# Kernel optimization log

Hardware: AMD Instinct MI355X
Metric: run time of the kernel (lower is better)

Reference implementation:

```python
import jax, jax.numpy as jnp
import numpy as np

OUT = 8192   # out_features
IN = 8192    # in_features
GS = 64      # HQQ group_size (axis=0 grouping)
NG = OUT * IN // GS   # number of quantization groups = 1048576
B = 64       # tokens in the batch


def setup_inputs() -> dict:
    key = jax.random.key(0)
    k1, k2, k3, k4, k5 = jax.random.split(key, 5)
    x = jax.random.normal(k1, (B, IN), dtype=jnp.float32)
    # packed 4-bit weights: two 4-bit values per byte, packed along axis 0
    # (HQQ pack_4bit_u8: packed = (W[:GS//2] << 4) | W[GS//2:])
    W_q = jax.random.randint(k2, (GS // 2, NG), 0, 256, dtype=jnp.int32)
    scale = jax.random.uniform(k3, (1, NG), dtype=jnp.float32, minval=0.001, maxval=0.02)
    zero = jax.random.uniform(k4, (1, NG), dtype=jnp.float32, minval=0.0, maxval=15.0)
    bias = jax.random.normal(k5, (OUT,), dtype=jnp.float32) * 0.01
    return {"x": x, "W_q": W_q, "scale": scale, "zero": zero, "bias": bias}


def reference(x, W_q, scale, zero, bias):
    # Unpack 4-bit: high nibble holds rows [0, GS//2), low nibble rows [GS//2, GS)
    hi = (W_q >> 4).astype(jnp.float32)          # (GS//2, NG)
    lo = (W_q & 0xF).astype(jnp.float32)         # (GS//2, NG)
    Wu = jnp.concatenate([hi, lo], axis=0)       # (GS, NG)
    # HQQ group-wise dequant: W = (W_q - zero) * scale, then reshape to (out, in)
    W = ((Wu - zero) * scale).reshape(OUT, IN)
    # linear: y = x @ W^T + bias
    return x @ W.T + bias
```

## Files before the change

### kernel.cpp

```cpp
#include <hip/hip_runtime.h>
#include <stdint.h>

#define OUT_F 8192
#define IN_F  8192
#define NGRP  1048576
#define BATCH 64
#define KS    4
#define NSTEP ((IN_F / KS) / 128)

typedef float f32x4  __attribute__((ext_vector_type(4)));
typedef float f32x16 __attribute__((ext_vector_type(16)));
typedef _Float16 half8_t __attribute__((ext_vector_type(8)));

static __device__ __forceinline__ unsigned int pk_fma_f16(unsigned int a, unsigned int b, unsigned int c) {
  unsigned int d;
  asm("v_pk_fma_f16 %0, %1, %2, %3" : "=v"(d) : "v"(a), "v"(b), "v"(c));
  return d;
}
static __device__ __forceinline__ unsigned int pk16(float a, float b) {
  unsigned short ua = __builtin_bit_cast(unsigned short, (_Float16)a);
  unsigned short ub = __builtin_bit_cast(unsigned short, (_Float16)b);
  return (unsigned int)ua | ((unsigned int)ub << 16);
}
static __device__ __forceinline__ unsigned int f2bf_pk(float a, float b) {
  unsigned ua = __builtin_bit_cast(unsigned, a);
  unsigned ub = __builtin_bit_cast(unsigned, b);
  ua = (ua + 0x7fffu + ((ua >> 16) & 1u)) >> 16;
  ub = (ub + 0x7fffu + ((ub >> 16) & 1u)) >> 16;
  return ua | (ub << 16);
}

#define GLL16(g, l)                                                         \
  __builtin_amdgcn_global_load_lds(                                         \
      (const __attribute__((address_space(1))) void*)(g),                   \
      (__attribute__((address_space(3))) void*)(l), 16, 0, 0)

__global__ __launch_bounds__(256) void pre_kernel(const float* __restrict__ x, ushort* __restrict__ xh,
                                                  const float* __restrict__ scale, const float* __restrict__ zero,
                                                  uint32_t* __restrict__ szb) {
  const int b = blockIdx.x;
  if (b < 512) {
    const int i = b * 256 + threadIdx.x;
    float4 v = ((const float4*)x)[i];
    ushort4 o;
    o.x = __builtin_bit_cast(unsigned short, (_Float16)v.x);
    o.y = __builtin_bit_cast(unsigned short, (_Float16)v.y);
    o.z = __builtin_bit_cast(unsigned short, (_Float16)v.z);
    o.w = __builtin_bit_cast(unsigned short, (_Float16)v.w);
    ((ushort4*)xh)[i] = o;
  } else {
    const int i = (b - 512) * 256 + threadIdx.x;
    float4 s = ((const float4*)scale)[i];
    float4 z = ((const float4*)zero)[i];
    uint4 o;
    o.x = pk16(s.x, s.y);
    o.y = pk16(-(64.f + z.x) * s.x, -(64.f + z.y) * s.y);
    o.z = pk16(s.z, s.w);
    o.w = pk16(-(64.f + z.z) * s.z, -(64.f + z.w) * s.w);
    ((uint4*)szb)[i] = o;
  }
}

__global__ __launch_bounds__(512, 4) void hqq_gemm_kernel(
    const int* __restrict__ Wq, const uint32_t* __restrict__ szb,
    const ushort* __restrict__ xh, ushort* __restrict__ partb)
{
  __shared__ ushort xlds[3][64 * 128];
  __shared__ ushort blds[2][64 * 128];

  const int t    = threadIdx.x;
  const int bid  = blockIdx.x;
  const int ks   = bid & 3;
  const int c    = bid >> 2;
  const int lane = t & 63;
  const int wid  = t >> 6;
  const int kbase = ks * (IN_F / KS);

  const int lr = t >> 5;
  const int i0 = (t & 31) * 4;
  const int* __restrict__ wq0 = Wq + (size_t)lr * NGRP + (size_t)c * IN_F + kbase + i0;
  const int* __restrict__ wq1 = wq0 + (size_t)16 * NGRP;
  const uint8_t* __restrict__ szp =
      (const uint8_t*)szb + ((size_t)c * IN_F + kbase + i0) * 4;
  const int wb0 = (i0 * 2) ^ ((lr & 7) << 4);

  const int kh   = wid & 1;
  const int mh   = (wid >> 1) & 1;
  const int nh   = wid >> 2;
  const int ln31 = lane & 31;
  const int koct = lane >> 5;
  const int arow = mh * 32 + ln31;
  const int brow = nh * 32 + ln31;

  f32x16 acc = {0.f, 0.f, 0.f, 0.f, 0.f, 0.f, 0.f, 0.f,
                0.f, 0.f, 0.f, 0.f, 0.f, 0.f, 0.f, 0.f};

  auto stage_x = [&](int bi, int s) {
    #pragma unroll
    for (int j = 0; j < 2; ++j) {
      const int m    = wid * 8 + j * 4 + (lane >> 4);
      const int scol = ((lane & 15) * 16) ^ ((m & 7) << 4);
      const ushort* g = xh + (size_t)m * IN_F + kbase + s * 128 + (scol >> 1);
      GLL16(g, &xlds[bi][(wid * 8 + j * 4) * 128]);
    }
  };

  auto ldregs = [&](int s, int4& w0, int4& w1, uint4& z4) {
    w0 = *(const int4*)(wq0 + (size_t)s * 128);
    w1 = *(const int4*)(wq1 + (size_t)s * 128);
    z4 = *(const uint4*)(szp + (size_t)s * 512);
  };

  auto stage_b = [&](int bi, const int4& w0, const int4& w1, const uint4& z4) {
    uint8_t* bb = (uint8_t*)&blds[bi][0];
    auto dqrow = [&](const int4& wv, int r) {
      unsigned tt0 = ((unsigned)wv.y << 16) | (unsigned)wv.x;
      unsigned tt1 = ((unsigned)wv.w << 16) | (unsigned)wv.z;
      uint2 hh, ll;
      hh.x = pk_fma_f16((tt0 & 0x00F000F0u) | 0x54005400u, z4.x, z4.y);
      hh.y = pk_fma_f16((tt1 & 0x00F000F0u) | 0x54005400u, z4.z, z4.w);
      ll.x = pk_fma_f16(((tt0 << 4) & 0x00F000F0u) | 0x54005400u, z4.x, z4.y);
      ll.y = pk_fma_f16(((tt1 << 4) & 0x00F000F0u) | 0x54005400u, z4.z, z4.w);
      *(uint2*)(bb + r * 256 + wb0)        = hh;
      *(uint2*)(bb + (r + 32) * 256 + wb0) = ll;
    };
    dqrow(w0, lr);
    dqrow(w1, lr + 16);
  };

  {
    int4 a0, a1; uint4 z0;
    ldregs(0, a0, a1, z0);
    stage_b(0, a0, a1, z0);
  }
  stage_x(0, 0);
  stage_x(1, 1);
  int4 w0, w1; uint4 z4;
  ldregs(1, w0, w1, z4);

  int xr0 = 0, xr1 = 1, xr2 = 2;

  #pragma unroll 1
  for (int s = 0; s < NSTEP; ++s) {
    asm volatile("s_waitcnt lgkmcnt(0)" ::: "memory");
    __builtin_amdgcn_s_barrier();

    const bool more2 = (s + 2 < NSTEP);
    int4 n0, n1; uint4 nz;
    if (more2) {
      stage_x(xr2, s + 2);
      ldregs(s + 2, n0, n1, nz);
    }

    if (more2)               asm volatile("s_waitcnt vmcnt(10)" ::: "memory");
    else if (s + 1 < NSTEP)  asm volatile("s_waitcnt vmcnt(5)" ::: "memory");
    else                     asm volatile("s_waitcnt vmcnt(0)" ::: "memory");
    __builtin_amdgcn_sched_barrier(0);

    const uint8_t* xb   = (const uint8_t*)&xlds[xr0][0];
    const uint8_t* bbuf = (const uint8_t*)&blds[s & 1][0];
    #pragma unroll
    for (int j = 0; j < 4; ++j) {
      const int kk   = kh * 4 + j;
      const int colb = (kk * 16 + koct * 8) * 2;
      half8_t a = *(const half8_t*)(xb   + arow * 256 + (colb ^ ((arow & 7) << 4)));
      half8_t b = *(const half8_t*)(bbuf + brow * 256 + (colb ^ ((brow & 7) << 4)));
      acc = __builtin_amdgcn_mfma_f32_32x32x16_f16(a, b, acc, 0, 0, 0);
    }

    if (s + 1 < NSTEP) stage_b((s + 1) & 1, w0, w1, z4);
    if (more2) { w0 = n0; w1 = n1; z4 = nz; }

    const int tmp = xr0; xr0 = xr1; xr1 = xr2; xr2 = tmp;
  }

  __syncthreads();
  float* red = (float*)&blds[0][0];
  {
    float4* dst = (float4*)(red + ((size_t)(wid * 64 + lane)) * 16);
    dst[0] = (float4){acc[0],  acc[1],  acc[2],  acc[3]};
    dst[1] = (float4){acc[4],  acc[5],  acc[6],  acc[7]};
    dst[2] = (float4){acc[8],  acc[9],  acc[10], acc[11]};
    dst[3] = (float4){acc[12], acc[13], acc[14], acc[15]};
  }
  __syncthreads();
  if (kh == 0) {
    const float4* src = (const float4*)(red + ((size_t)((wid ^ 1) * 64 + lane)) * 16);
    float4 p0 = src[0], p1 = src[1], p2 = src[2], p3 = src[3];
    const int o = ln31 * 128 + c + nh * 4096;
    const int mbase = mh * 32 + 4 * koct;
    ushort* bp = partb + ((size_t)ks * OUT_F + o) * BATCH + mbase;
    uint2 q;
    q.x = f2bf_pk(acc[0]  + p0.x, acc[1]  + p0.y);
    q.y = f2bf_pk(acc[2]  + p0.z, acc[3]  + p0.w);
    *(uint2*)(bp + 0) = q;
    q.x = f2bf_pk(acc[4]  + p1.x, acc[5]  + p1.y);
    q.y = f2bf_pk(acc[6]  + p1.z, acc[7]  + p1.w);
    *(uint2*)(bp + 8) = q;
    q.x = f2bf_pk(acc[8]  + p2.x, acc[9]  + p2.y);
    q.y = f2bf_pk(acc[10] + p2.z, acc[11] + p2.w);
    *(uint2*)(bp + 16) = q;
    q.x = f2bf_pk(acc[12] + p3.x, acc[13] + p3.y);
    q.y = f2bf_pk(acc[14] + p3.z, acc[15] + p3.w);
    *(uint2*)(bp + 24) = q;
  }
}

__global__ __launch_bounds__(256) void reduce_kernel(const ushort* __restrict__ partb,
                                                     const float* __restrict__ bias,
                                                     float* __restrict__ out)
{
  __shared__ float tile[32][65];
  const int ob = blockIdx.x;
  const int t  = threadIdx.x;
  {
    const int ol = t >> 3;
    const int mg = t & 7;
    const int o  = ob * 32 + ol;
    const size_t base = (size_t)o * BATCH + mg * 8;
    float s[8] = {0, 0, 0, 0, 0, 0, 0, 0};
    #pragma unroll
    for (int ks = 0; ks < KS; ++ks) {
      const ushort* p = partb + (size_t)ks * OUT_F * BATCH + base;
      uint4 v = *(const uint4*)p;
      s[0] += __uint_as_float(v.x << 16); s[1] += __uint_as_float(v.x & 0xffff0000u);
      s[2] += __uint_as_float(v.y << 16); s[3] += __uint_as_float(v.y & 0xffff0000u);
      s[4] += __uint_as_float(v.z << 16); s[5] += __uint_as_float(v.z & 0xffff0000u);
      s[6] += __uint_as_float(v.w << 16); s[7] += __uint_as_float(v.w & 0xffff0000u);
    }
    const float bv = bias[o];
    #pragma unroll
    for (int j = 0; j < 8; ++j) tile[ol][mg * 8 + j] = s[j] + bv;
  }
  __syncthreads();
  {
    const int m  = t >> 2;
    const int og = (t & 3) * 8;
    float r[8];
    #pragma unroll
    for (int j = 0; j < 8; ++j) r[j] = tile[og + j][m];
    float* op = out + (size_t)m * OUT_F + ob * 32 + og;
    *(float4*)op       = (float4){r[0], r[1], r[2], r[3]};
    *(float4*)(op + 4) = (float4){r[4], r[5], r[6], r[7]};
  }
}

__global__ void hqq_fallback_kernel(const float* __restrict__ x, const int* __restrict__ Wq,
                                    const float* __restrict__ scale, const float* __restrict__ zero,
                                    const float* __restrict__ bias, float* __restrict__ out)
{
  int idx = blockIdx.x * blockDim.x + threadIdx.x;
  int b = idx >> 13;
  int o = idx & 8191;
  int g = o >> 7, cc = o & 127;
  int r = g & 31;
  bool hi = (g < 32);
  const int*   wrow = Wq    + (size_t)r  * NGRP + (size_t)cc * IN_F;
  const float* srow = scale + (size_t)cc * IN_F;
  const float* zrow = zero  + (size_t)cc * IN_F;
  const float* xrow = x     + (size_t)b  * IN_F;
  float acc = 0.f;
  for (int k = 0; k < IN_F; ++k) {
    int v = wrow[k];
    float nib = (float)(hi ? (v >> 4) : (v & 15));
    acc += xrow[k] * ((nib - zrow[k]) * srow[k]);
  }
  out[idx] = acc + bias[o];
}

extern "C" void kernel_launch(void* const* d_in, const int* in_sizes, int n_in,
                              void* d_out, int out_size, void* d_ws, size_t ws_size,
                              hipStream_t stream) {
  const float* x     = (const float*)d_in[0];
  const int*   Wq    = (const int*)d_in[1];
  const float* scale = (const float*)d_in[2];
  const float* zero  = (const float*)d_in[3];
  const float* bias  = (const float*)d_in[4];
  float* out = (float*)d_out;

  const size_t xh_bytes   = (size_t)BATCH * IN_F * sizeof(ushort);
  const size_t sz_bytes   = (size_t)NGRP * 4;
  const size_t part_bytes = (size_t)KS * BATCH * OUT_F * sizeof(ushort);

  if (ws_size >= xh_bytes + sz_bytes + part_bytes) {
    ushort*   xh    = (ushort*)d_ws;
    uint32_t* szb   = (uint32_t*)((char*)d_ws + xh_bytes);
    ushort*   partb = (ushort*)((char*)d_ws + xh_bytes + sz_bytes);
    pre_kernel<<<1536, 256, 0, stream>>>(x, xh, scale, zero, szb);
    hqq_gemm_kernel<<<128 * KS, 512, 0, stream>>>(Wq, szb, xh, partb);
    reduce_kernel<<<OUT_F / 32, 256, 0, stream>>>(partb, bias, out);
  } else {
    hqq_fallback_kernel<<<(BATCH * OUT_F) / 256, 256, 0, stream>>>(x, Wq, scale, zero, bias, out);
  }
}
```

Before: 40.19 us.

## Load activation MFMA operands directly from global into registers instead of LDS

```diff
diff --git a/kernel.cpp b/kernel.cpp
--- a/kernel.cpp
+++ b/kernel.cpp
@@ -29,11 +29,6 @@
   ub = (ub + 0x7fffu + ((ub >> 16) & 1u)) >> 16;
   return ua | (ub << 16);
 }
-
-#define GLL16(g, l)                                                         \
-  __builtin_amdgcn_global_load_lds(                                         \
-      (const __attribute__((address_space(1))) void*)(g),                   \
-      (__attribute__((address_space(3))) void*)(l), 16, 0, 0)
 
 __global__ __launch_bounds__(256) void pre_kernel(const float* __restrict__ x, ushort* __restrict__ xh,
                                                   const float* __restrict__ scale, const float* __restrict__ zero,
@@ -65,7 +60,6 @@
     const int* __restrict__ Wq, const uint32_t* __restrict__ szb,
     const ushort* __restrict__ xh, ushort* __restrict__ partb)
 {
-  __shared__ ushort xlds[3][64 * 128];
   __shared__ ushort blds[2][64 * 128];
 
   const int t    = threadIdx.x;
@@ -89,21 +83,12 @@
   const int nh   = wid >> 2;
   const int ln31 = lane & 31;
   const int koct = lane >> 5;
-  const int arow = mh * 32 + ln31;
   const int brow = nh * 32 + ln31;
+  const ushort* __restrict__ xap =
+      xh + (size_t)(mh * 32 + ln31) * IN_F + kbase + kh * 64 + koct * 8;
 
   f32x16 acc = {0.f, 0.f, 0.f, 0.f, 0.f, 0.f, 0.f, 0.f,
                 0.f, 0.f, 0.f, 0.f, 0.f, 0.f, 0.f, 0.f};
-
-  auto stage_x = [&](int bi, int s) {
-    #pragma unroll
-    for (int j = 0; j < 2; ++j) {
-      const int m    = wid * 8 + j * 4 + (lane >> 4);
-      const int scol = ((lane & 15) * 16) ^ ((m & 7) << 4);
-      const ushort* g = xh + (size_t)m * IN_F + kbase + s * 128 + (scol >> 1);
-      GLL16(g, &xlds[bi][(wid * 8 + j * 4) * 128]);
-    }
-  };
 
   auto ldregs = [&](int s, int4& w0, int4& w1, uint4& z4) {
     w0 = *(const int4*)(wq0 + (size_t)s * 128);
@@ -133,45 +118,47 @@
     ldregs(0, a0, a1, z0);
     stage_b(0, a0, a1, z0);
   }
-  stage_x(0, 0);
-  stage_x(1, 1);
   int4 w0, w1; uint4 z4;
   ldregs(1, w0, w1, z4);
-
-  int xr0 = 0, xr1 = 1, xr2 = 2;
+  half8_t a0 = *(const half8_t*)(xap);
+  half8_t a1 = *(const half8_t*)(xap + 16);
+  half8_t a2 = *(const half8_t*)(xap + 32);
+  half8_t a3 = *(const half8_t*)(xap + 48);
 
   #pragma unroll 1
   for (int s = 0; s < NSTEP; ++s) {
     asm volatile("s_waitcnt lgkmcnt(0)" ::: "memory");
     __builtin_amdgcn_s_barrier();
 
+    const bool more1 = (s + 1 < NSTEP);
     const bool more2 = (s + 2 < NSTEP);
+    half8_t m0, m1, m2, m3;
     int4 n0, n1; uint4 nz;
-    if (more2) {
-      stage_x(xr2, s + 2);
-      ldregs(s + 2, n0, n1, nz);
+    if (more1) {
+      const ushort* xs = xap + (size_t)(s + 1) * 128;
+      m0 = *(const half8_t*)(xs);
+      m1 = *(const half8_t*)(xs + 16);
+      m2 = *(const half8_t*)(xs + 32);
+      m3 = *(const half8_t*)(xs + 48);
     }
-
-    if (more2)               asm volatile("s_waitcnt vmcnt(10)" ::: "memory");
-    else if (s + 1 < NSTEP)  asm volatile("s_waitcnt vmcnt(5)" ::: "memory");
-    else                     asm volatile("s_waitcnt vmcnt(0)" ::: "memory");
-    __builtin_amdgcn_sched_barrier(0);
-
-    const uint8_t* xb   = (const uint8_t*)&xlds[xr0][0];
+    if (more2) ldregs(s + 2, n0, n1, nz);
+
     const uint8_t* bbuf = (const uint8_t*)&blds[s & 1][0];
-    #pragma unroll
-    for (int j = 0; j < 4; ++j) {
-      const int kk   = kh * 4 + j;
-      const int colb = (kk * 16 + koct * 8) * 2;
-      half8_t a = *(const half8_t*)(xb   + arow * 256 + (colb ^ ((arow & 7) << 4)));
-      half8_t b = *(const half8_t*)(bbuf + brow * 256 + (colb ^ ((brow & 7) << 4)));
-      acc = __builtin_amdgcn_mfma_f32_32x32x16_f16(a, b, acc, 0, 0, 0);
+    {
+      const int colb = (kh * 64 + koct * 8) * 2;
+      half8_t b = *(const half8_t*)(bbuf + brow * 256 + ((colb +  0) ^ ((brow & 7) << 4)));
+      acc = __builtin_amdgcn_mfma_f32_32x32x16_f16(a0, b, acc, 0, 0, 0);
+      b = *(const half8_t*)(bbuf + brow * 256 + ((colb + 32) ^ ((brow & 7) << 4)));
+      acc = __builtin_amdgcn_mfma_f32_32x32x16_f16(a1, b, acc, 0, 0, 0);
+      b = *(const half8_t*)(bbuf + brow * 256 + ((colb + 64) ^ ((brow & 7) << 4)));
+      acc = __builtin_amdgcn_mfma_f32_32x32x16_f16(a2, b, acc, 0, 0, 0);
+      b = *(const half8_t*)(bbuf + brow * 256 + ((colb + 96) ^ ((brow & 7) << 4)));
+      acc = __builtin_amdgcn_mfma_f32_32x32x16_f16(a3, b, acc, 0, 0, 0);
     }
 
-    if (s + 1 < NSTEP) stage_b((s + 1) & 1, w0, w1, z4);
+    if (more1) stage_b((s + 1) & 1, w0, w1, z4);
+    if (more1) { a0 = m0; a1 = m1; a2 = m2; a3 = m3; }
     if (more2) { w0 = n0; w1 = n1; z4 = nz; }
-
-    const int tmp = xr0; xr0 = xr1; xr1 = xr2; xr2 = tmp;
   }
 
   __syncthreads();
```

Result: slower. 56.25 us (+40.0%).
